# Kernel optimization log

Measured on AMD Instinct MI355X. Metric: run time of the kernel, lower is better.

The kernel has to match this reference:

```python
import jax, jax.numpy as jnp
import numpy as np

SEQ_LS = [512, 512, 512, 512]
HEADS = 8
DIM_HEAD = 64
DIM = 512
INNER = HEADS * DIM_HEAD  # 512
N = sum(SEQ_LS)           # 2048
B = 4
EPS = 1e-5

# static modality id per token position: [N]
MOD_IDS = jnp.asarray(np.repeat(np.arange(len(SEQ_LS)), SEQ_LS))


def setup_inputs() -> dict:
    key = jax.random.key(0)
    ks = jax.random.split(key, 6)
    x = jax.random.normal(ks[0], (B, N, DIM), dtype=jnp.float32)
    m_labels = jnp.ones((B, len(SEQ_LS)), dtype=jnp.int64 if jax.config.jax_enable_x64 else jnp.int32)
    gamma = jnp.ones((DIM,), dtype=jnp.float32)
    beta = jnp.zeros((DIM,), dtype=jnp.float32)
    w_qkv = jax.random.normal(ks[1], (DIM, 3 * INNER), dtype=jnp.float32) * (DIM ** -0.5)
    w_out = jax.random.normal(ks[2], (INNER, DIM), dtype=jnp.float32) * (INNER ** -0.5)
    b_out = jnp.zeros((DIM,), dtype=jnp.float32)
    return {"x": x, "m_labels": m_labels, "gamma": gamma, "beta": beta,
            "w_qkv": w_qkv, "w_out": w_out, "b_out": b_out}


def _additive_mask(m_labels):
    # present[b, n] = modality of token n is present in sample b
    present = (m_labels[:, MOD_IDS] != 0)                       # [B, N] bool
    pair_ok = present[:, :, None] & present[:, None, :]         # [B, N, N]
    neg_inf = jnp.float32(-jnp.inf)
    return jnp.where(pair_ok, jnp.float32(0.0), neg_inf)        # [B, N, N]


def reference(x, m_labels, gamma, beta, w_qkv, w_out, b_out):
    # LayerNorm(dim)
    mu = jnp.mean(x, axis=-1, keepdims=True)
    var = jnp.mean(jnp.square(x - mu), axis=-1, keepdims=True)
    xn = (x - mu) * jax.lax.rsqrt(var + EPS) * gamma + beta

    # QKV projection (no bias), split heads
    qkv = jnp.einsum('bnd,de->bne', xn, w_qkv)                  # [B, N, 3*INNER]
    q, k, v = jnp.split(qkv, 3, axis=-1)
    def heads(t):
        return t.reshape(B, N, HEADS, DIM_HEAD).transpose(0, 2, 1, 3)  # [B, H, N, Dh]
    q, k, v = heads(q), heads(k), heads(v)

    scale = DIM_HEAD ** -0.5
    dots = jnp.einsum('bhnd,bhmd->bhnm', q, k) * scale          # [B, H, N, N]
    dots = dots + _additive_mask(m_labels)[:, None, :, :]
    attn = jax.nn.softmax(dots, axis=-1)
    out = jnp.einsum('bhnm,bhmd->bhnd', attn, v)                # [B, H, N, Dh]
    out = out.transpose(0, 2, 1, 3).reshape(B, N, INNER)        # [B, N, INNER]
    return jnp.einsum('bni,io->bno', out, w_out) + b_out        # [B, N, DIM]
```

## Files before the change

kernel.cpp:

```cpp
#include <hip/hip_runtime.h>

#define DIMD 512
#define NTOK 2048
#define HEADS 8
#define DH 64

typedef __attribute__((ext_vector_type(4))) float f32x4;
typedef __attribute__((ext_vector_type(8))) __bf16 bf16x8;
typedef __attribute__((ext_vector_type(4))) short s16x4;

#define MFMA16(a, b, c) __builtin_amdgcn_mfma_f32_16x16x32_bf16((a), (b), (c), 0, 0, 0)
#define MFMAK16(a, b, c) __builtin_amdgcn_mfma_f32_16x16x16bf16_1k((a), (b), (c), 0, 0, 0)

__device__ __forceinline__ unsigned short f2bf(float f) {
  unsigned int u = __float_as_uint(f);
  u += 0x7fffu + ((u >> 16) & 1u);
  return (unsigned short)(u >> 16);
}

__device__ __forceinline__ unsigned packhi(float b, float a) {
#if __has_builtin(__builtin_amdgcn_perm)
  return __builtin_amdgcn_perm(__float_as_uint(a), __float_as_uint(b), 0x07060302u);
#else
  return (__float_as_uint(b) >> 16) | (__float_as_uint(a) & 0xffff0000u);
#endif
}

__device__ __forceinline__ void gl2lds16(const void* g, void* l) {
  auto gp = reinterpret_cast<__attribute__((address_space(1))) unsigned int*>(
      reinterpret_cast<unsigned long long>(g));
  auto lp = reinterpret_cast<__attribute__((address_space(3))) unsigned int*>(
      reinterpret_cast<unsigned long long>(l));
  __builtin_amdgcn_global_load_lds(gp, lp, 16, 0, 0);
}

__global__ __launch_bounds__(256) void prep_kernel(const float* __restrict__ x,
                                                   const float* __restrict__ gamma,
                                                   const float* __restrict__ beta,
                                                   const float* __restrict__ w_qkv,
                                                   const float* __restrict__ w_out,
                                                   unsigned short* __restrict__ xn,
                                                   unsigned short* __restrict__ wqkvT,
                                                   unsigned short* __restrict__ woutT) {
  __shared__ float t[32][33];
  const int bid = blockIdx.x;
  if (bid < 2048) {
    const int row = bid * 4 + (threadIdx.x >> 6);
    const int lane = threadIdx.x & 63;
    const float4* xr = (const float4*)(x + (size_t)row * DIMD);
    float4 a = xr[lane];
    float4 b = xr[lane + 64];
    float s = a.x + a.y + a.z + a.w + b.x + b.y + b.z + b.w;
    for (int off = 1; off < 64; off <<= 1) s += __shfl_xor(s, off, 64);
    float mu = s * (1.0f / DIMD);
    float d0 = a.x - mu, d1 = a.y - mu, d2 = a.z - mu, d3 = a.w - mu;
    float e0 = b.x - mu, e1 = b.y - mu, e2 = b.z - mu, e3 = b.w - mu;
    float v = d0 * d0 + d1 * d1 + d2 * d2 + d3 * d3 + e0 * e0 + e1 * e1 + e2 * e2 + e3 * e3;
    for (int off = 1; off < 64; off <<= 1) v += __shfl_xor(v, off, 64);
    float rs = rsqrtf(v * (1.0f / DIMD) + 1e-5f);
    const float4* g4 = (const float4*)gamma;
    const float4* be4 = (const float4*)beta;
    float4 ga = g4[lane], gb = g4[lane + 64];
    float4 ba = be4[lane], bb = be4[lane + 64];
    unsigned p0 = (unsigned)f2bf(d0 * rs * ga.x + ba.x) | ((unsigned)f2bf(d1 * rs * ga.y + ba.y) << 16);
    unsigned p1 = (unsigned)f2bf(d2 * rs * ga.z + ba.z) | ((unsigned)f2bf(d3 * rs * ga.w + ba.w) << 16);
    unsigned p2 = (unsigned)f2bf(e0 * rs * gb.x + bb.x) | ((unsigned)f2bf(e1 * rs * gb.y + bb.y) << 16);
    unsigned p3 = (unsigned)f2bf(e2 * rs * gb.z + bb.z) | ((unsigned)f2bf(e3 * rs * gb.w + bb.w) << 16);
    uint2 w0; w0.x = p0; w0.y = p1;
    uint2 w1; w1.x = p2; w1.y = p3;
    *(uint2*)&xn[(size_t)row * DIMD + lane * 4] = w0;
    *(uint2*)&xn[(size_t)row * DIMD + 256 + lane * 4] = w1;
  } else {
    const float* w;
    unsigned short* wt;
    int C, bx, by;
    if (bid < 2816) { w = w_qkv; wt = wqkvT; C = 1536; bx = (bid - 2048) % 48; by = (bid - 2048) / 48; }
    else            { w = w_out; wt = woutT; C = 512;  bx = (bid - 2816) % 16; by = (bid - 2816) / 16; }
    const int R = 512;
    int tx = threadIdx.x & 31, ty = threadIdx.x >> 5;
    int c0 = bx * 32, r0 = by * 32;
    for (int i = 0; i < 4; i++)
      t[ty + 8 * i][tx] = w[(size_t)(r0 + ty + 8 * i) * C + c0 + tx];
    __syncthreads();
    for (int i = 0; i < 4; i++)
      wt[(size_t)(c0 + ty + 8 * i) * R + r0 + tx] = f2bf(t[tx][ty + 8 * i]);
  }
}

__global__ __launch_bounds__(256, 2) void qkv_gemm(const unsigned short* __restrict__ A,
                                                   const unsigned short* __restrict__ Bt,
                                                   unsigned short* __restrict__ qb,
                                                   unsigned short* __restrict__ kb,
                                                   unsigned short* __restrict__ vtb) {
  __shared__ unsigned short As[2][128 * 64];
  __shared__ unsigned short Bs[2][128 * 64];
  const int tid = threadIdx.x;
  const int wave = tid >> 6, lane = tid & 63;
  const int row16 = lane & 15, quad = lane >> 4;
  const int rho = row16 & 7;
  const int m0 = blockIdx.x * 128;
  const int n0 = blockIdx.y * 128;
  const int rw = (wave & 1) * 64, cw = (wave >> 1) * 64;

  const char* Ab = (const char*)A;
  const char* Bb = (const char*)Bt;
#pragma unroll
  for (int i = 0; i < 4; i++) {
    int idx = i * 256 + tid;
    int r = idx >> 3;
    int c = (idx & 7) ^ (r & 7);
    gl2lds16(Ab + ((size_t)(m0 + r) * DIMD) * 2 + c * 16, (char*)As[0] + idx * 16);
    gl2lds16(Bb + ((size_t)(n0 + r) * DIMD) * 2 + c * 16, (char*)Bs[0] + idx * 16);
  }
  __syncthreads();

  f32x4 acc[4][4] = {};
  for (int kt = 0; kt < 8; kt++) {
    const int buf = kt & 1;
    if (kt < 7) {
      const int k0 = (kt + 1) * 64;
#pragma unroll
      for (int i = 0; i < 4; i++) {
        int idx = i * 256 + tid;
        int r = idx >> 3;
        int c = (idx & 7) ^ (r & 7);
        gl2lds16(Ab + ((size_t)(m0 + r) * DIMD + k0) * 2 + c * 16, (char*)As[buf ^ 1] + idx * 16);
        gl2lds16(Bb + ((size_t)(n0 + r) * DIMD + k0) * 2 + c * 16, (char*)Bs[buf ^ 1] + idx * 16);
      }
    }
#pragma unroll
    for (int ks = 0; ks < 2; ks++) {
      bf16x8 av[4], bv[4];
#pragma unroll
      for (int i = 0; i < 4; i++) {
        int Ra = rw + i * 16 + row16;
        int Rb = cw + i * 16 + row16;
        av[i] = *(const bf16x8*)&As[buf][Ra * 64 + (((ks * 4 + quad) ^ rho) * 8)];
        bv[i] = *(const bf16x8*)&Bs[buf][Rb * 64 + (((ks * 4 + quad) ^ rho) * 8)];
      }
#pragma unroll
      for (int i = 0; i < 4; i++)
#pragma unroll
        for (int j = 0; j < 4; j++) acc[i][j] = MFMA16(av[i], bv[j], acc[i][j]);
    }
    __syncthreads();
  }

  unsigned short* Ct = (unsigned short*)As;
#pragma unroll
  for (int i = 0; i < 4; i++)
#pragma unroll
    for (int j = 0; j < 4; j++)
#pragma unroll
      for (int r = 0; r < 4; r++)
        Ct[(rw + i * 16 + quad * 4 + r) * 136 + cw + j * 16 + row16] = f2bf(acc[i][j][r]);
  __syncthreads();

  const int sect = n0 >> 9;
  const int h0 = (n0 & 511) >> 6;
  const int b = m0 >> 11;
  const int nbase = m0 & 2047;
  if (sect < 2) {
    unsigned short* dst = (sect == 0) ? qb : kb;
#pragma unroll
    for (int i = 0; i < 8; i++) {
      int cid = i * 256 + tid;
      int row = cid >> 4, col0 = (cid & 15) * 8;
      int h = h0 + (col0 >> 6), d0 = col0 & 63;
      uint4 val = *(const uint4*)&Ct[row * 136 + col0];
      *(uint4*)&dst[(((size_t)(b * HEADS + h) * NTOK) + nbase + row) * DH + d0] = val;
    }
  } else {
#pragma unroll
    for (int u = 0; u < 4; u++) {
      int uid = u * 256 + tid;
      int col = uid >> 3, rc = (uid & 7) * 16;
      int h = h0 + (col >> 6), d = col & 63;
      unsigned short tmp[16];
#pragma unroll
      for (int j = 0; j < 16; j++) tmp[j] = Ct[(rc + j) * 136 + col];
      size_t base = ((size_t)(b * HEADS + h) * DH + d) * NTOK + nbase + rc;
      *(uint4*)&vtb[base] = *(uint4*)&tmp[0];
      *(uint4*)&vtb[base + 8] = *(uint4*)&tmp[8];
    }
  }
}

__global__ __launch_bounds__(256, 2) void attn_kernel(const unsigned short* __restrict__ qb,
                                                      const unsigned short* __restrict__ kb,
                                                      const unsigned short* __restrict__ vtb,
                                                      const int* __restrict__ mlab,
                                                      unsigned short* __restrict__ ao) {
  __shared__ unsigned short Qs[128 * 64];
  __shared__ unsigned short Ks[2][64 * 64];
  __shared__ unsigned short Vs[2][64 * 64];
  const int tid = threadIdx.x;
  const int wave = tid >> 6, lane = tid & 63;
  const int row16 = lane & 15, quad = lane >> 4;
  const int rho = row16 & 7;
  const int bh = blockIdx.y;
  const int b = bh >> 3, h = bh & 7;
  const int q0 = blockIdx.x * 128;

  const char* qg = (const char*)(qb + ((size_t)bh * NTOK + q0) * DH);
  const char* kgb = (const char*)(kb + (size_t)bh * NTOK * DH);
  const char* vgb = (const char*)(vtb + (size_t)bh * DH * NTOK);
  const int sr = tid >> 3;
  const int sc = (tid & 7) ^ (sr & 7);

#pragma unroll
  for (int i = 0; i < 4; i++)
    gl2lds16(qg + (sr + 32 * i) * 128 + sc * 16, (char*)Qs + tid * 16 + i * 4096);
  gl2lds16(kgb + sr * 128 + sc * 16, (char*)Ks[0] + tid * 16);
  gl2lds16(kgb + (sr + 32) * 128 + sc * 16, (char*)Ks[0] + tid * 16 + 4096);
  gl2lds16(vgb + (size_t)sr * 4096 + sc * 16, (char*)Vs[0] + tid * 16);
  gl2lds16(vgb + (size_t)(sr + 32) * 4096 + sc * 16, (char*)Vs[0] + tid * 16 + 4096);
  __syncthreads();

  bf16x8 aq[2][2];
#pragma unroll
  for (int qs = 0; qs < 2; qs++) {
    const int qrow = wave * 32 + qs * 16 + row16;
#pragma unroll
    for (int ki = 0; ki < 2; ki++)
      aq[qs][ki] = *(const bf16x8*)&Qs[qrow * 64 + (((ki * 4 + quad) ^ rho) * 8)];
  }

  s16x4 onesf;
  onesf[0] = onesf[1] = onesf[2] = onesf[3] = (short)0x3F80;

  f32x4 accT[4][2] = {};
  f32x4 accL[2] = {};
  const float cs = 0.125f * 1.44269504088896f;
  const float c0 = mlab[b * 4 + 0] ? -16.f : -100000.f;
  const float c1 = mlab[b * 4 + 1] ? -16.f : -100000.f;
  const float c2 = mlab[b * 4 + 2] ? -16.f : -100000.f;
  const float c3 = mlab[b * 4 + 3] ? -16.f : -100000.f;

  for (int t = 0; t < 32; t++) {
    const int buf = t & 1;
    if (t < 31) {
      const char* kg = kgb + (size_t)(t + 1) * 8192;
      char* lk = (char*)Ks[buf ^ 1];
      gl2lds16(kg + sr * 128 + sc * 16, lk + tid * 16);
      gl2lds16(kg + (sr + 32) * 128 + sc * 16, lk + tid * 16 + 4096);
      const char* vg = vgb + (size_t)(t + 1) * 128;
      char* lv = (char*)Vs[buf ^ 1];
      gl2lds16(vg + (size_t)sr * 4096 + sc * 16, lv + tid * 16);
      gl2lds16(vg + (size_t)(sr + 32) * 4096 + sc * 16, lv + tid * 16 + 4096);
    }
    f32x4 S[2][4];
#pragma unroll
    for (int f = 0; f < 4; f++) {
      const unsigned short* Kr = &Ks[buf][(f * 16 + row16) * 64];
      bf16x8 ak0 = *(const bf16x8*)&Kr[(quad ^ rho) * 8];
      bf16x8 ak1 = *(const bf16x8*)&Kr[((quad + 4) ^ rho) * 8];
#pragma unroll
      for (int qs = 0; qs < 2; qs++) {
        f32x4 z = {};
        z = MFMA16(ak0, aq[qs][0], z);
        z = MFMA16(ak1, aq[qs][1], z);
        S[qs][f] = z;
      }
    }
    const int mi = t >> 3;
    const float c = (mi == 0) ? c0 : (mi == 1) ? c1 : (mi == 2) ? c2 : c3;
    s16x4 pf[2][4];
#pragma unroll
    for (int qs = 0; qs < 2; qs++)
#pragma unroll
      for (int f = 0; f < 4; f++) {
        float p0 = exp2f(fmaf(S[qs][f][0], cs, c));
        float p1 = exp2f(fmaf(S[qs][f][1], cs, c));
        float p2 = exp2f(fmaf(S[qs][f][2], cs, c));
        float p3 = exp2f(fmaf(S[qs][f][3], cs, c));
        uint2 pk;
        pk.x = packhi(p0, p1);
        pk.y = packhi(p2, p3);
        pf[qs][f] = *(s16x4*)&pk;
      }
#pragma unroll
    for (int g = 0; g < 4; g++) {
      const unsigned short* Vr = &Vs[buf][(g * 16 + row16) * 64];
#pragma unroll
      for (int u = 0; u < 4; u++) {
        s16x4 va = *(const s16x4*)&Vr[(((2 * u + (quad >> 1)) ^ rho) * 8) + (quad & 1) * 4];
#pragma unroll
        for (int qs = 0; qs < 2; qs++) accT[g][qs] = MFMAK16(va, pf[qs][u], accT[g][qs]);
      }
    }
#pragma unroll
    for (int u = 0; u < 4; u++)
#pragma unroll
      for (int qs = 0; qs < 2; qs++) accL[qs] = MFMAK16(onesf, pf[qs][u], accL[qs]);
    __syncthreads();
  }

  float inv[2];
  inv[0] = 1.0f / accL[0][0];
  inv[1] = 1.0f / accL[1][0];
#pragma unroll
  for (int qs = 0; qs < 2; qs++) {
    const int q = q0 + wave * 32 + qs * 16 + row16;
    unsigned short* aor = ao + ((size_t)b * NTOK + q) * DIMD + h * DH;
#pragma unroll
    for (int g = 0; g < 4; g++) {
      *(unsigned*)&aor[g * 16 + quad * 4] = packhi(accT[g][qs][0] * inv[qs], accT[g][qs][1] * inv[qs]);
      *(unsigned*)&aor[g * 16 + quad * 4 + 2] = packhi(accT[g][qs][2] * inv[qs], accT[g][qs][3] * inv[qs]);
    }
  }
}

__global__ __launch_bounds__(256, 2) void out_gemm(const unsigned short* __restrict__ A,
                                                   const unsigned short* __restrict__ Bt,
                                                   const float* __restrict__ bias,
                                                   float* __restrict__ out) {
  __shared__ unsigned short As[2][128 * 64];
  __shared__ unsigned short Bs[2][64 * 64];
  const int tid = threadIdx.x;
  const int wave = tid >> 6, lane = tid & 63;
  const int row16 = lane & 15, quad = lane >> 4;
  const int rho = row16 & 7;
  const int m0 = blockIdx.x * 128;
  const int n0 = blockIdx.y * 64;
  const int rw = (wave & 1) * 64, cw = (wave >> 1) * 32;

  const char* Ab = (const char*)A;
  const char* Bb = (const char*)Bt;
#pragma unroll
  for (int i = 0; i < 4; i++) {
    int idx = i * 256 + tid;
    int r = idx >> 3;
    int c = (idx & 7) ^ (r & 7);
    gl2lds16(Ab + ((size_t)(m0 + r) * DIMD) * 2 + c * 16, (char*)As[0] + idx * 16);
  }
#pragma unroll
  for (int i = 0; i < 2; i++) {
    int idx = i * 256 + tid;
    int r = idx >> 3;
    int c = (idx & 7) ^ (r & 7);
    gl2lds16(Bb + ((size_t)(n0 + r) * DIMD) * 2 + c * 16, (char*)Bs[0] + idx * 16);
  }
  __syncthreads();

  f32x4 acc[4][2] = {};
  for (int kt = 0; kt < 8; kt++) {
    const int buf = kt & 1;
    if (kt < 7) {
      const int k0 = (kt + 1) * 64;
#pragma unroll
      for (int i = 0; i < 4; i++) {
        int idx = i * 256 + tid;
        int r = idx >> 3;
        int c = (idx & 7) ^ (r & 7);
        gl2lds16(Ab + ((size_t)(m0 + r) * DIMD + k0) * 2 + c * 16, (char*)As[buf ^ 1] + idx * 16);
      }
#pragma unroll
      for (int i = 0; i < 2; i++) {
        int idx = i * 256 + tid;
        int r = idx >> 3;
        int c = (idx & 7) ^ (r & 7);
        gl2lds16(Bb + ((size_t)(n0 + r) * DIMD + k0) * 2 + c * 16, (char*)Bs[buf ^ 1] + idx * 16);
      }
    }
#pragma unroll
    for (int ks = 0; ks < 2; ks++) {
      bf16x8 av[4], bv[2];
#pragma unroll
      for (int i = 0; i < 4; i++)
        av[i] = *(const bf16x8*)&As[buf][(rw + i * 16 + row16) * 64 + (((ks * 4 + quad) ^ rho) * 8)];
#pragma unroll
      for (int j = 0; j < 2; j++)
        bv[j] = *(const bf16x8*)&Bs[buf][(cw + j * 16 + row16) * 64 + (((ks * 4 + quad) ^ rho) * 8)];
#pragma unroll
      for (int i = 0; i < 4; i++)
#pragma unroll
        for (int j = 0; j < 2; j++) acc[i][j] = MFMA16(av[i], bv[j], acc[i][j]);
    }
    __syncthreads();
  }

#pragma unroll
  for (int j = 0; j < 2; j++) {
    const int col = n0 + cw + j * 16 + row16;
    const float bv = bias[col];
#pragma unroll
    for (int i = 0; i < 4; i++)
#pragma unroll
      for (int r = 0; r < 4; r++) {
        const int row = m0 + rw + i * 16 + quad * 4 + r;
        out[(size_t)row * DIMD + col] = acc[i][j][r] + bv;
      }
  }
}

extern "C" void kernel_launch(void* const* d_in, const int* in_sizes, int n_in,
                              void* d_out, int out_size, void* d_ws, size_t ws_size,
                              hipStream_t stream) {
  const float* x = (const float*)d_in[0];
  const int* mlab = (const int*)d_in[1];
  const float* gamma = (const float*)d_in[2];
  const float* beta = (const float*)d_in[3];
  const float* w_qkv = (const float*)d_in[4];
  const float* w_out = (const float*)d_in[5];
  const float* b_out = (const float*)d_in[6];
  float* out = (float*)d_out;

  char* ws = (char*)d_ws;
  unsigned short* xn = (unsigned short*)(ws);
  unsigned short* wqkvT = (unsigned short*)(ws + 8388608);
  unsigned short* woutT = (unsigned short*)(ws + 9961472);
  unsigned short* qbuf = (unsigned short*)(ws + 10485760);
  unsigned short* kbuf = (unsigned short*)(ws + 18874368);
  unsigned short* vtbuf = (unsigned short*)(ws + 27262976);
  unsigned short* aobuf = (unsigned short*)(ws + 35651584);

  prep_kernel<<<3072, 256, 0, stream>>>(x, gamma, beta, w_qkv, w_out, xn, wqkvT, woutT);
  qkv_gemm<<<dim3(64, 12), 256, 0, stream>>>(xn, wqkvT, qbuf, kbuf, vtbuf);
  attn_kernel<<<dim3(16, 32), 256, 0, stream>>>(qbuf, kbuf, vtbuf, mlab, aobuf);
  out_gemm<<<dim3(64, 8), 256, 0, stream>>>(aobuf, woutT, b_out, out);
}
```

Before: 170.2 us.

## Double attention query tile to 256 rows with 8 waves and sum rows with VALU

The attention kernel now runs 512 threads per block, each block covering 256 query rows, so every K/V tile loaded into LDS is reused by twice as many waves and each thread issues half as many loads. The row-sum for softmax normalization moves from extra MFMAs against a ones vector to scalar adds of the probabilities plus a cross-lane shuffle reduction. The grid halves to 256 blocks, which lowers the number of blocks in flight per CU. The sum is now taken from fp32 probabilities rather than their bf16-rounded values.

```diff
diff --git a/kernel.cpp b/kernel.cpp
--- a/kernel.cpp
+++ b/kernel.cpp
@@ -186,12 +186,12 @@
   }
 }
 
-__global__ __launch_bounds__(256, 2) void attn_kernel(const unsigned short* __restrict__ qb,
-                                                      const unsigned short* __restrict__ kb,
-                                                      const unsigned short* __restrict__ vtb,
-                                                      const int* __restrict__ mlab,
-                                                      unsigned short* __restrict__ ao) {
-  __shared__ unsigned short Qs[128 * 64];
+__global__ __launch_bounds__(512) void attn_kernel(const unsigned short* __restrict__ qb,
+                                                   const unsigned short* __restrict__ kb,
+                                                   const unsigned short* __restrict__ vtb,
+                                                   const int* __restrict__ mlab,
+                                                   unsigned short* __restrict__ ao) {
+  __shared__ unsigned short Qs[256 * 64];
   __shared__ unsigned short Ks[2][64 * 64];
   __shared__ unsigned short Vs[2][64 * 64];
   const int tid = threadIdx.x;
@@ -200,7 +200,7 @@
   const int rho = row16 & 7;
   const int bh = blockIdx.y;
   const int b = bh >> 3, h = bh & 7;
-  const int q0 = blockIdx.x * 128;
+  const int q0 = blockIdx.x * 256;
 
   const char* qg = (const char*)(qb + ((size_t)bh * NTOK + q0) * DH);
   const char* kgb = (const char*)(kb + (size_t)bh * NTOK * DH);
@@ -210,11 +210,9 @@
 
 #pragma unroll
   for (int i = 0; i < 4; i++)
-    gl2lds16(qg + (sr + 32 * i) * 128 + sc * 16, (char*)Qs + tid * 16 + i * 4096);
+    gl2lds16(qg + (sr + 64 * i) * 128 + sc * 16, (char*)Qs + tid * 16 + i * 8192);
   gl2lds16(kgb + sr * 128 + sc * 16, (char*)Ks[0] + tid * 16);
-  gl2lds16(kgb + (sr + 32) * 128 + sc * 16, (char*)Ks[0] + tid * 16 + 4096);
   gl2lds16(vgb + (size_t)sr * 4096 + sc * 16, (char*)Vs[0] + tid * 16);
-  gl2lds16(vgb + (size_t)(sr + 32) * 4096 + sc * 16, (char*)Vs[0] + tid * 16 + 4096);
   __syncthreads();
 
   bf16x8 aq[2][2];
@@ -226,11 +224,8 @@
       aq[qs][ki] = *(const bf16x8*)&Qs[qrow * 64 + (((ki * 4 + quad) ^ rho) * 8)];
   }
 
-  s16x4 onesf;
-  onesf[0] = onesf[1] = onesf[2] = onesf[3] = (short)0x3F80;
-
   f32x4 accT[4][2] = {};
-  f32x4 accL[2] = {};
+  float lsum[2] = {0.f, 0.f};
   const float cs = 0.125f * 1.44269504088896f;
   const float c0 = mlab[b * 4 + 0] ? -16.f : -100000.f;
   const float c1 = mlab[b * 4 + 1] ? -16.f : -100000.f;
@@ -240,14 +235,8 @@
   for (int t = 0; t < 32; t++) {
     const int buf = t & 1;
     if (t < 31) {
-      const char* kg = kgb + (size_t)(t + 1) * 8192;
-      char* lk = (char*)Ks[buf ^ 1];
-      gl2lds16(kg + sr * 128 + sc * 16, lk + tid * 16);
-      gl2lds16(kg + (sr + 32) * 128 + sc * 16, lk + tid * 16 + 4096);
-      const char* vg = vgb + (size_t)(t + 1) * 128;
-      char* lv = (char*)Vs[buf ^ 1];
-      gl2lds16(vg + (size_t)sr * 4096 + sc * 16, lv + tid * 16);
-      gl2lds16(vg + (size_t)(sr + 32) * 4096 + sc * 16, lv + tid * 16 + 4096);
+      gl2lds16(kgb + (size_t)(t + 1) * 8192 + sr * 128 + sc * 16, (char*)Ks[buf ^ 1] + tid * 16);
+      gl2lds16(vgb + (size_t)(t + 1) * 128 + (size_t)sr * 4096 + sc * 16, (char*)Vs[buf ^ 1] + tid * 16);
     }
     f32x4 S[2][4];
 #pragma unroll
@@ -274,6 +263,7 @@
         float p1 = exp2f(fmaf(S[qs][f][1], cs, c));
         float p2 = exp2f(fmaf(S[qs][f][2], cs, c));
         float p3 = exp2f(fmaf(S[qs][f][3], cs, c));
+        lsum[qs] += (p0 + p1) + (p2 + p3);
         uint2 pk;
         pk.x = packhi(p0, p1);
         pk.y = packhi(p2, p3);
@@ -289,24 +279,24 @@
         for (int qs = 0; qs < 2; qs++) accT[g][qs] = MFMAK16(va, pf[qs][u], accT[g][qs]);
       }
     }
-#pragma unroll
-    for (int u = 0; u < 4; u++)
-#pragma unroll
-      for (int qs = 0; qs < 2; qs++) accL[qs] = MFMAK16(onesf, pf[qs][u], accL[qs]);
     __syncthreads();
   }
 
-  float inv[2];
-  inv[0] = 1.0f / accL[0][0];
-  inv[1] = 1.0f / accL[1][0];
+#pragma unroll
+  for (int qs = 0; qs < 2; qs++) {
+    float s = lsum[qs];
+    s += __shfl_xor(s, 16, 64);
+    s += __shfl_xor(s, 32, 64);
+    lsum[qs] = 1.0f / s;
+  }
 #pragma unroll
   for (int qs = 0; qs < 2; qs++) {
     const int q = q0 + wave * 32 + qs * 16 + row16;
     unsigned short* aor = ao + ((size_t)b * NTOK + q) * DIMD + h * DH;
 #pragma unroll
     for (int g = 0; g < 4; g++) {
-      *(unsigned*)&aor[g * 16 + quad * 4] = packhi(accT[g][qs][0] * inv[qs], accT[g][qs][1] * inv[qs]);
-      *(unsigned*)&aor[g * 16 + quad * 4 + 2] = packhi(accT[g][qs][2] * inv[qs], accT[g][qs][3] * inv[qs]);
+      *(unsigned*)&aor[g * 16 + quad * 4] = packhi(accT[g][qs][0] * lsum[qs], accT[g][qs][1] * lsum[qs]);
+      *(unsigned*)&aor[g * 16 + quad * 4 + 2] = packhi(accT[g][qs][2] * lsum[qs], accT[g][qs][3] * lsum[qs]);
     }
   }
 }
@@ -417,6 +407,6 @@
 
   prep_kernel<<<3072, 256, 0, stream>>>(x, gamma, beta, w_qkv, w_out, xn, wqkvT, woutT);
   qkv_gemm<<<dim3(64, 12), 256, 0, stream>>>(xn, wqkvT, qbuf, kbuf, vtbuf);
-  attn_kernel<<<dim3(16, 32), 256, 0, stream>>>(qbuf, kbuf, vtbuf, mlab, aobuf);
+  attn_kernel<<<dim3(8, 32), 512, 0, stream>>>(qbuf, kbuf, vtbuf, mlab, aobuf);
   out_gemm<<<dim3(64, 8), 256, 0, stream>>>(aobuf, woutT, b_out, out);
 }
```

After: 166.6 us. 1.02x faster.
